# Kernel optimization log

Hardware: AMD Instinct MI355X
Metric: run time of the kernel (lower is better)

## Reference

```python
import jax, jax.numpy as jnp
import numpy as np

NY = NX = 512
DX = DY = 200.0
RHO, G, FD = 910.0, 9.81, 1e-16
TTOT, DTMAX = 200.0, 1.0
EPS = 1e-10
T_FREQ = 5.0
LAPSE = 0.006        # degC per m, lapse rate used by assumed update_smb
MELT = 0.5           # m/yr per degC, degree-day melt factor
N_STEPS = 400        # fixed upper bound on while-loop iterations (dt<=1yr, ttot=200yr)
N_PRECIP = 64


def _make_squash(scale):
    # identity in forward; backward applies atan(scale*g)/scale (torch register_hook)
    @jax.custom_vjp
    def f(x):
        return x
    def fwd(x):
        return x, None
    def bwd(_, g):
        return (jnp.arctan(scale * g) / scale,)
    f.defvjp(fwd, bwd)
    return f

squash_smb = _make_squash(0.51)   # reduce_hook
squash_zs = _make_squash(0.051)   # reduce_hook2


def update_smb(Z_surf, precip, T_m_lowest, T_s):
    # degree-day surface mass balance (update_smb not present in source excerpt)
    T = T_m_lowest[0] + T_s[0] - LAPSE * Z_surf
    return precip - MELT * jnp.maximum(T, 0.0)


def setup_inputs() -> dict:
    key = jax.random.key(0)
    k1, = jax.random.split(key, 1)
    # smooth synthetic mountain topography (Gaussian bump, 3000 m peak)
    y = np.linspace(-1.0, 1.0, NY, dtype=np.float32)
    x = np.linspace(-1.0, 1.0, NX, dtype=np.float32)
    xx, yy = np.meshgrid(x, y)
    Z_topo = jnp.asarray(3000.0 * np.exp(-(xx ** 2 + yy ** 2) / 0.3), dtype=jnp.float32)
    precip_tensor = 2.0 * jax.random.uniform(k1, (N_PRECIP, NY, NX), dtype=jnp.float32)
    T_m_lowest = jnp.array([5.0], dtype=jnp.float32)
    T_s = jnp.array([2.0], dtype=jnp.float32)
    return {"Z_topo": Z_topo, "precip_tensor": precip_tensor,
            "T_m_lowest": T_m_lowest, "T_s": T_s}


def _solve(Z_topo, precip_tensor, T_m_lowest, T_s):
    H = jnp.zeros((NY, NX), jnp.float32)
    Zs = Z_topo + H
    smb = update_smb(Zs, precip_tensor[0], T_m_lowest, T_s)
    zero2d = jnp.zeros((NY, NX), jnp.float32)
    carry0 = (H, Zs, smb, jnp.float32(0.0), jnp.int32(0), jnp.float32(0.0),
              zero2d, zero2d, jnp.bool_(False), jnp.bool_(False))

    def step(carry, _):
        H, Zs, smb, time, idx, t_last, H1, H2, s1, s2 = carry
        active = time < TTOT
        # staggered-grid SIA stencil
        H_avg = 0.25 * (H[:-1, :-1] + H[1:, 1:] + H[:-1, 1:] + H[1:, :-1])
        Sx = (Zs[:, 1:] - Zs[:, :-1]) / DX
        Sy = (Zs[1:, :] - Zs[:-1, :]) / DY
        Sx = 0.5 * (Sx[:-1, :] + Sx[1:, :])
        Sy = 0.5 * (Sy[:, :-1] + Sy[:, 1:])
        Snorm = jnp.sqrt(Sx ** 2 + Sy ** 2 + EPS)
        D = FD * (RHO * G) ** 3 * H_avg ** 5 * Snorm ** 2 + EPS   # (ny-1, nx-1)
        # dt via .item() in torch -> detached constant
        dt = jax.lax.stop_gradient(
            jnp.minimum(min(DX, DY) ** 2 / (2.7 * jnp.max(D)), DTMAX))
        dt = jnp.where(active, dt, jnp.float32(0.0))  # no-op once ttot reached
        qx = -(0.5 * (D[:-1, :] + D[1:, :])) * (Zs[1:-1, 1:] - Zs[1:-1, :-1]) / DX
        qy = -(0.5 * (D[:, :-1] + D[:, 1:])) * (Zs[1:, 1:-1] - Zs[:-1, 1:-1]) / DY
        dHdt = -(jnp.diff(qx, axis=1) / DX + jnp.diff(qy, axis=0) / DY)  # (ny-2, nx-2)
        smb_sq = squash_smb(smb)
        H = H.at[1:-1, 1:-1].add(dt * (dHdt + smb_sq[1:-1, 1:-1]))
        H = jax.nn.relu(H)
        Zs = squash_zs(Z_topo + H)
        time = time + dt
        cap1 = jnp.logical_and(jnp.logical_not(s1), time >= 120.0)
        H1 = jnp.where(cap1, jax.lax.stop_gradient(H), H1)
        s1 = jnp.logical_or(s1, cap1)
        cap2 = jnp.logical_and(jnp.logical_not(s2), time >= 160.0)
        H2 = jnp.where(cap2, jax.lax.stop_gradient(H), H2)
        s2 = jnp.logical_or(s2, cap2)
        do_upd = jnp.logical_and(active, (time - t_last) >= T_FREQ)
        idx = jnp.where(do_upd, jnp.minimum(idx + 1, N_PRECIP - 1), idx)
        smb_new = update_smb(Zs, precip_tensor[idx], T_m_lowest, T_s)
        smb = jnp.where(do_upd, smb_new, smb)
        t_last = jnp.where(do_upd, time, t_last)
        return (H, Zs, smb, time, idx, t_last, H1, H2, s1, s2), None

    carry, _ = jax.lax.scan(jax.checkpoint(step), carry0, None, length=N_STEPS)
    H, Zs, smb, time, idx, t_last, H1, H2, s1, s2 = carry
    return H1, H2, H


def reference(Z_topo, precip_tensor, T_m_lowest, T_s):
    return _solve(Z_topo, precip_tensor, T_m_lowest, T_s)
```

## Files before the change

### kernel.cpp

```cpp
#include <hip/hip_runtime.h>
#include <math.h>


#define NN 512
#define MM (NN * NN)
#define NSTEPS 400
#define NW 128
#define HR 4
#define TPB 512

typedef unsigned long long ull;

__device__ __forceinline__ ull ald(const ull* p) {
  return __hip_atomic_load(p, __ATOMIC_RELAXED, __HIP_MEMORY_SCOPE_AGENT);
}
__device__ __forceinline__ void asto(ull* p, ull v) {
  __hip_atomic_store(p, v, __ATOMIC_RELAXED, __HIP_MEMORY_SCOPE_AGENT);
}
__device__ __forceinline__ ull lld(const ull* p) {
  return __hip_atomic_load(p, __ATOMIC_RELAXED, __HIP_MEMORY_SCOPE_WORKGROUP);
}
__device__ __forceinline__ void lst(ull* p, ull v) {
  __hip_atomic_store(p, v, __ATOMIC_RELAXED, __HIP_MEMORY_SCOPE_WORKGROUP);
}

__global__ __launch_bounds__(TPB)
void glacier_kernel(const float* __restrict__ Zt,
                    const float* __restrict__ precip,
                    const float* __restrict__ Tm,
                    const float* __restrict__ Ts,
                    float* __restrict__ out,
                    ull* __restrict__ ring,
                    ull* __restrict__ halo) {
  __shared__ float Zs2[2][HR + 4][NN];
  __shared__ float DB[HR + 3][NN];
  __shared__ float HnB[HR + 2][NN];
  __shared__ ull gm[2];
  __shared__ unsigned lmx[2], lcnt[2];

  ull* upH = halo;
  ull* upD = halo + 2 * NW * NN;
  ull* dnH = halo + 4 * NW * NN;
  ull* dnD = halo + 6 * NW * NN;

  const int w = blockIdx.x;
  const int j = threadIdx.x;
  const int lane = j & 63;
  const int a = w * HR;
  const bool hasT = (w > 0), hasB = (w < NW - 1);
  const float TmTs = Tm[0] + Ts[0];
  const double RG = 910.0 * 9.81;
  const float CDIF = (float)(1e-16 * RG * RG * RG);
  const float C_Q = 1.25e-5f;
  const float C_S2 = 6.25e-6f;
  const size_t wofs = (size_t)w * NN;

  float ztreg[HR + 4];
  float hcur[HR + 2];
  float smbreg[HR + 2];

#pragma unroll
  for (int ls = 0; ls < HR + 4; ++ls) {
    int r = a - 2 + ls;
    float zt = (r >= 0 && r < NN) ? Zt[r * NN + j] : 0.f;
    ztreg[ls] = zt;
    Zs2[0][ls][j] = zt;
  }
#pragma unroll
  for (int ln = 0; ln < HR + 2; ++ln) {
    int r = a - 1 + ln;
    hcur[ln] = 0.f;
    float sm = 0.f;
    if (r >= 0 && r < NN) {
      float T = TmTs - 0.006f * ztreg[ln + 1];
      sm = precip[r * NN + j] - 0.5f * fmaxf(T, 0.f);
    }
    smbreg[ln] = sm;
  }
#pragma unroll
  for (int ld = 0; ld < HR + 3; ++ld) DB[ld][j] = 1e-10f;
#pragma unroll
  for (int rr = 0; rr < HR; ++rr) {
    int id = (a + rr) * NN + j;
    out[id] = 0.f;
    out[MM + id] = 0.f;
  }
  if (j == 0) { lmx[0] = 0u; lmx[1] = 0u; lcnt[0] = 0u; lcnt[1] = 0u;
                gm[0] = 0ull; gm[1] = 0ull; }
  float zs0r = ztreg[0], zs7r = ztreg[HR + 3];
  float d0r = 1e-10f, d6r = 1e-10f;
  const ull initD = (ull)__float_as_uint(1e-10f);
  __syncthreads();

  float time = 0.f, t_last = 0.f;
  int idx = 0;
  bool s1 = false, s2 = false;

  for (int k = 0; k < NSTEPS; ++k) {
    if (time >= 200.0f) break;

    const int p = k & 1;
    const size_t pc = (size_t)(k & 1) * NW * NN;
    const size_t pn = (size_t)((k + 1) & 1) * NW * NN;
    const ull tg = ((ull)(unsigned)(k + 1)) << 32;
    ull* ringp = ring + (size_t)(k & 1) * NW * 16;

    if (j == 0) { lmx[(k + 1) & 1] = 0u; lcnt[(k + 1) & 1] = 0u; }

    bool pre = (time - t_last) >= 4.0f;
    int idxn = min(idx + 1, 63);
    float pf[HR + 2];
    if (pre) {
      const float* prowN = precip + (size_t)idxn * MM;
#pragma unroll
      for (int ln = 0; ln < HR + 2; ++ln) {
        int i = a - 1 + ln;
        pf[ln] = (i >= 0 && i < NN) ? prowN[i * NN + j] : 0.f;
      }
    } else {
#pragma unroll
      for (int ln = 0; ln < HR + 2; ++ln) pf[ln] = 0.f;
    }
    const ull *pHt = nullptr, *pDt = nullptr, *pHb = nullptr, *pDb = nullptr;
    const ull *pDtm = nullptr, *pDbm = nullptr;
    ull vHt = 0, vDt = 0, vHb = 0, vDb = 0;
    ull vDtm = initD, vDbm = initD;
    const ull* gp = nullptr; ull gv = 0;
    if (k > 0) {
      if (hasT) {
        pHt = dnH + pc + (size_t)(w - 1) * NN + j;
        pDt = dnD + pc + (size_t)(w - 1) * NN + j;
        vHt = ald(pHt);
        if (j < NN - 1) vDt = ald(pDt);
        if (lane == 0 && j > 0) { pDtm = dnD + pc + (size_t)(w - 1) * NN + (j - 1); vDtm = ald(pDtm); }
      }
      if (hasB) {
        pHb = upH + pc + (size_t)(w + 1) * NN + j;
        pDb = upD + pc + (size_t)(w + 1) * NN + j;
        vHb = ald(pHb);
        if (j < NN - 1) vDb = ald(pDb);
        if (lane == 0 && j > 0) { pDbm = upD + pc + (size_t)(w + 1) * NN + (j - 1); vDbm = ald(pDbm); }
      }
      if (j < NW) { gp = ringp + j * 16; gv = ald(gp); }
    }
    asm volatile("" ::: "memory");

    float dHdt[HR + 2];
#pragma unroll
    for (int ln = 1; ln <= HR; ++ln) {
      int i = a - 1 + ln;
      float v = 0.f;
      if (i > 0 && i < NN - 1 && j > 0 && j < NN - 1) {
        int li = ln + 1;
        float zc = Zs2[p][li][j];
        float zw = Zs2[p][li][j - 1];
        float ze = Zs2[p][li][j + 1];
        float zn = Zs2[p][li - 1][j];
        float zs_ = Zs2[p][li + 1][j];
        float d00 = DB[ln][j - 1], d01 = DB[ln][j];
        float d10 = DB[ln + 1][j - 1], d11 = DB[ln + 1][j];
        v = C_Q * (((d01 + d11) * (ze - zc) - (d00 + d10) * (zc - zw)) +
                   ((d10 + d11) * (zs_ - zc) - (d00 + d01) * (zc - zn)));
      }
      dHdt[ln] = v;
    }

    if (k > 0) {
      if (pHt) {
        while ((unsigned)(vHt >> 32) < (unsigned)k) {
          __builtin_amdgcn_s_sleep(1); vHt = ald(pHt);
        }
        if (j < NN - 1)
          while ((unsigned)(vDt >> 32) < (unsigned)k) {
            __builtin_amdgcn_s_sleep(1); vDt = ald(pDt);
          }
        if (pDtm)
          while ((unsigned)(vDtm >> 32) < (unsigned)k) {
            __builtin_amdgcn_s_sleep(1); vDtm = ald(pDtm);
          }
        zs0r = ztreg[0] + __uint_as_float((unsigned)vHt);
        if (j < NN - 1) d0r = __uint_as_float((unsigned)vDt);
      }
      if (pHb) {
        while ((unsigned)(vHb >> 32) < (unsigned)k) {
          __builtin_amdgcn_s_sleep(1); vHb = ald(pHb);
        }
        if (j < NN - 1)
          while ((unsigned)(vDb >> 32) < (unsigned)k) {
            __builtin_amdgcn_s_sleep(1); vDb = ald(pDb);
          }
        if (pDbm)
          while ((unsigned)(vDbm >> 32) < (unsigned)k) {
            __builtin_amdgcn_s_sleep(1); vDbm = ald(pDbm);
          }
        zs7r = ztreg[HR + 3] + __uint_as_float((unsigned)vHb);
        if (j < NN - 1) d6r = __uint_as_float((unsigned)vDb);
      }
      if (j < NW) {
        while ((unsigned)(gv >> 32) < (unsigned)k) {
          __builtin_amdgcn_s_sleep(1); gv = ald(gp);
        }
        float lm = __uint_as_float((unsigned)gv);
        for (int off = 32; off; off >>= 1) lm = fmaxf(lm, __shfl_xor(lm, off));
        if (lane == 0)
          lst(&gm[j >> 6], ((ull)(unsigned)k << 32) | (ull)__float_as_uint(lm));
      }
    }

    {
      float dW0 = __shfl_up(d0r, 1);
      float dW6 = __shfl_up(d6r, 1);
      if (lane == 0) {
        dW0 = __uint_as_float((unsigned)vDtm);
        dW6 = __uint_as_float((unsigned)vDbm);
      }
      int i0 = a - 1;
      float v0 = 0.f;
      if (i0 > 0 && i0 < NN - 1 && j > 0 && j < NN - 1) {
        float zc = Zs2[p][1][j], zw = Zs2[p][1][j - 1], ze = Zs2[p][1][j + 1];
        float zn = zs0r, zs_ = Zs2[p][2][j];
        float d00 = dW0, d01 = d0r;
        float d10 = DB[1][j - 1], d11 = DB[1][j];
        v0 = C_Q * (((d01 + d11) * (ze - zc) - (d00 + d10) * (zc - zw)) +
                    ((d10 + d11) * (zs_ - zc) - (d00 + d01) * (zc - zn)));
      }
      dHdt[0] = v0;
      int i5 = a + HR;
      float v5 = 0.f;
      if (i5 > 0 && i5 < NN - 1 && j > 0 && j < NN - 1) {
        float zc = Zs2[p][HR + 2][j], zw = Zs2[p][HR + 2][j - 1], ze = Zs2[p][HR + 2][j + 1];
        float zn = Zs2[p][HR + 1][j], zs_ = zs7r;
        float d00 = DB[HR + 1][j - 1], d01 = DB[HR + 1][j];
        float d10 = dW6, d11 = d6r;
        v5 = C_Q * (((d01 + d11) * (ze - zc) - (d00 + d10) * (zc - zw)) +
                    ((d10 + d11) * (zs_ - zc) - (d00 + d01) * (zc - zn)));
      }
      dHdt[HR + 1] = v5;
    }

    float sd[HR + 2];
#pragma unroll
    for (int ln = 0; ln < HR + 2; ++ln) sd[ln] = dHdt[ln] + smbreg[ln];

    float maxD;
    if (k == 0) {
      maxD = 1e-10f;
    } else {
      ull g0 = lld(&gm[0]);
      while ((unsigned)(g0 >> 32) < (unsigned)k) {
        __builtin_amdgcn_s_sleep(1); g0 = lld(&gm[0]);
      }
      ull g1 = lld(&gm[1]);
      while ((unsigned)(g1 >> 32) < (unsigned)k) {
        __builtin_amdgcn_s_sleep(1); g1 = lld(&gm[1]);
      }
      maxD = fmaxf(__uint_as_float((unsigned)g0),
                   __uint_as_float((unsigned)g1));
    }
    float dt = fminf(40000.0f / (2.7f * maxD), 1.0f);
    float tnew = time + dt;
    bool cap1 = (!s1) && (tnew >= 120.0f);
    bool cap2 = (!s2) && (tnew >= 160.0f);
    bool do_upd = (tnew - t_last) >= 5.0f;

    float hnxt[HR + 2];
#pragma unroll
    for (int ln = 0; ln < HR + 2; ++ln) {
      int i = a - 1 + ln;
      float hnew = 0.f;
      if (i >= 0 && i < NN) {
        if (i > 0 && i < NN - 1 && j > 0 && j < NN - 1)
          hnew = fmaxf(fmaf(dt, sd[ln], hcur[ln]), 0.f);
        float zsn = ztreg[ln + 1] + hnew;
        HnB[ln][j] = hnew;
        Zs2[p ^ 1][ln + 1][j] = zsn;
        if (ln == 2) asto(upH + pn + wofs + j, tg | (ull)__float_as_uint(hnew));
        if (ln == 3) asto(dnH + pn + wofs + j, tg | (ull)__float_as_uint(hnew));
        if (i >= a && i < a + HR) {
          int id = i * NN + j;
          if (cap1) out[id] = hnew;
          if (cap2) out[MM + id] = hnew;
        }
        if (do_upd)
          smbreg[ln] = pf[ln] - 0.5f * fmaxf(TmTs - 0.006f * zsn, 0.f);
      }
      hnxt[ln] = hnew;
    }
    __syncthreads();

    float lmax = 0.f;
#pragma unroll
    for (int ln = 0; ln < HR + 1; ++ln) {
      int r = a - 1 + ln;
      if (r >= 0 && r < NN - 1 && j < NN - 1) {
        float h00 = HnB[ln][j], h01 = HnB[ln][j + 1];
        float h10 = HnB[ln + 1][j], h11 = HnB[ln + 1][j + 1];
        float z00 = Zs2[p ^ 1][ln + 1][j], z01 = Zs2[p ^ 1][ln + 1][j + 1];
        float z10 = Zs2[p ^ 1][ln + 2][j], z11 = Zs2[p ^ 1][ln + 2][j + 1];
        float havg = 0.25f * (((h00 + h11) + h01) + h10);
        float u = (z01 - z00) + (z11 - z10);
        float vv = (z10 - z00) + (z11 - z01);
        float s2 = C_S2 * (u * u + vv * vv) + 1e-10f;
        float h2 = havg * havg;
        float h4 = h2 * h2;
        float h5 = h4 * havg;
        float d = CDIF * h5 * s2 + 1e-10f;
        DB[ln + 1][j] = d;
        if (ln == 1) asto(upD + pn + wofs + j, tg | (ull)__float_as_uint(d));
        if (ln == 3) asto(dnD + pn + wofs + j, tg | (ull)__float_as_uint(d));
        lmax = fmaxf(lmax, d);
      }
    }
    for (int off = 32; off; off >>= 1) lmax = fmaxf(lmax, __shfl_xor(lmax, off));
    if (lane == 0) {
      atomicMax(&lmx[k & 1], __float_as_uint(lmax));
      unsigned c = atomicAdd(&lcnt[k & 1], 1u);
      if (c == 7u) {
        unsigned mv = atomicAdd(&lmx[k & 1], 0u);
        asto(ring + (size_t)((k + 1) & 1) * NW * 16 + w * 16,
             ((ull)(unsigned)(k + 1) << 32) | (ull)mv);
      }
    }

#pragma unroll
    for (int ln = 0; ln < HR + 2; ++ln) hcur[ln] = hnxt[ln];
    time = tnew;
    s1 = s1 || cap1;
    s2 = s2 || cap2;
    if (do_upd) { idx = idxn; t_last = tnew; }
    __syncthreads();
  }

#pragma unroll
  for (int rr = 0; rr < HR; ++rr)
    out[2 * MM + (a + rr) * NN + j] = hcur[rr + 1];
}

extern "C" void kernel_launch(void* const* d_in, const int* in_sizes, int n_in,
                              void* d_out, int out_size, void* d_ws, size_t ws_size,
                              hipStream_t stream) {
  const float* Zt = (const float*)d_in[0];
  const float* precip = (const float*)d_in[1];
  const float* Tm = (const float*)d_in[2];
  const float* Ts = (const float*)d_in[3];
  float* out = (float*)d_out;

  ull* ring = (ull*)d_ws;
  ull* halo = (ull*)((char*)d_ws + 32768);

  hipMemsetAsync(d_ws, 0, 32768 + (size_t)8 * NW * NN * sizeof(ull), stream);
  glacier_kernel<<<NW, TPB, 0, stream>>>(Zt, precip, Tm, Ts, out, ring, halo);
}
```

Baseline: 1.272 ms.

## Split each row band across two blocks with column ghost exchange

Each 4-row band is now handled by two 256-thread blocks, each owning half the columns, so the persistent kernel runs 256 blocks instead of 128 and spreads across more compute units. The blocks trade left and right ghost columns of H and D through tagged global flags with spin-waits, and the global max reduction now reads 256 ring entries. This adds cross-block synchronisation on the critical path each step, and the specL thread must wait for its neighbour's H before computing D.

```diff
diff --git a/kernel.cpp b/kernel.cpp
--- a/kernel.cpp
+++ b/kernel.cpp
@@ -5,9 +5,10 @@
 #define NN 512
 #define MM (NN * NN)
 #define NSTEPS 400
-#define NW 128
+#define NBANDS 128
+#define NBLK 256
 #define HR 4
-#define TPB 512
+#define TPB 256
 
 typedef unsigned long long ull;
 
@@ -22,6 +23,11 @@
 }
 __device__ __forceinline__ void lst(ull* p, ull v) {
   __hip_atomic_store(p, v, __ATOMIC_RELAXED, __HIP_MEMORY_SCOPE_WORKGROUP);
+}
+__device__ __forceinline__ float spinf(const ull* p, unsigned kk) {
+  ull v = ald(p);
+  while ((unsigned)(v >> 32) < kk) { __builtin_amdgcn_s_sleep(1); v = ald(p); }
+  return __uint_as_float((unsigned)v);
 }
 
 __global__ __launch_bounds__(TPB)
@@ -31,23 +37,33 @@
                     const float* __restrict__ Ts,
                     float* __restrict__ out,
                     ull* __restrict__ ring,
-                    ull* __restrict__ halo) {
-  __shared__ float Zs2[2][HR + 4][NN];
-  __shared__ float DB[HR + 3][NN];
-  __shared__ float HnB[HR + 2][NN];
-  __shared__ ull gm[2];
+                    ull* __restrict__ halo,
+                    ull* __restrict__ ghost) {
+  __shared__ float Zs2[2][HR + 4][256];
+  __shared__ float DB[HR + 3][256];
+  __shared__ float HnB[HR + 2][256];
+  __shared__ ull gm[4];
   __shared__ unsigned lmx[2], lcnt[2];
 
   ull* upH = halo;
-  ull* upD = halo + 2 * NW * NN;
-  ull* dnH = halo + 4 * NW * NN;
-  ull* dnD = halo + 6 * NW * NN;
-
-  const int w = blockIdx.x;
+  ull* upD = halo + 2 * NBANDS * NN;
+  ull* dnH = halo + 4 * NBANDS * NN;
+  ull* dnD = halo + 6 * NBANDS * NN;
+  ull* gHL = ghost;
+  ull* gDL = ghost + 2 * NBANDS * 8;
+  ull* gHR = ghost + 4 * NBANDS * 8;
+
+  const int w = blockIdx.x >> 1;
+  const int half = blockIdx.x & 1;
   const int j = threadIdx.x;
+  const int jg = (half << 8) | j;
   const int lane = j & 63;
+  const int jm = (j > 0) ? j - 1 : 0;
+  const int jp = (j < 255) ? j + 1 : 255;
   const int a = w * HR;
-  const bool hasT = (w > 0), hasB = (w < NW - 1);
+  const bool hasT = (w > 0), hasB = (w < NBANDS - 1);
+  const bool specR = (half == 1) && (j == 0);
+  const bool specL = (half == 0) && (j == 255);
   const float TmTs = Tm[0] + Ts[0];
   const double RG = 910.0 * 9.81;
   const float CDIF = (float)(1e-16 * RG * RG * RG);
@@ -62,7 +78,7 @@
 #pragma unroll
   for (int ls = 0; ls < HR + 4; ++ls) {
     int r = a - 2 + ls;
-    float zt = (r >= 0 && r < NN) ? Zt[r * NN + j] : 0.f;
+    float zt = (r >= 0 && r < NN) ? Zt[r * NN + jg] : 0.f;
     ztreg[ls] = zt;
     Zs2[0][ls][j] = zt;
   }
@@ -73,7 +89,7 @@
     float sm = 0.f;
     if (r >= 0 && r < NN) {
       float T = TmTs - 0.006f * ztreg[ln + 1];
-      sm = precip[r * NN + j] - 0.5f * fmaxf(T, 0.f);
+      sm = precip[r * NN + jg] - 0.5f * fmaxf(T, 0.f);
     }
     smbreg[ln] = sm;
   }
@@ -81,15 +97,26 @@
   for (int ld = 0; ld < HR + 3; ++ld) DB[ld][j] = 1e-10f;
 #pragma unroll
   for (int rr = 0; rr < HR; ++rr) {
-    int id = (a + rr) * NN + j;
+    int id = (a + rr) * NN + jg;
     out[id] = 0.f;
     out[MM + id] = 0.f;
   }
   if (j == 0) { lmx[0] = 0u; lmx[1] = 0u; lcnt[0] = 0u; lcnt[1] = 0u;
-                gm[0] = 0ull; gm[1] = 0ull; }
+                gm[0] = 0ull; gm[1] = 0ull; gm[2] = 0ull; gm[3] = 0ull; }
   float zs0r = ztreg[0], zs7r = ztreg[HR + 3];
   float d0r = 1e-10f, d6r = 1e-10f;
   const ull initD = (ull)__float_as_uint(1e-10f);
+  float gzt[6], gzs[6], gd[5];
+  float rzt[6], rzs[6];
+#pragma unroll
+  for (int r = 0; r < 6; ++r) {
+    int row = a - 1 + r;
+    float ztL = (specR && row >= 0 && row < NN) ? Zt[row * NN + 255] : 0.f;
+    float ztR = (specL && row >= 0 && row < NN) ? Zt[row * NN + 256] : 0.f;
+    gzt[r] = ztL; gzs[r] = ztL;
+    rzt[r] = ztR; rzs[r] = ztR;
+    if (r < 5) gd[r] = 1e-10f;
+  }
   __syncthreads();
 
   float time = 0.f, t_last = 0.f;
@@ -100,10 +127,12 @@
     if (time >= 200.0f) break;
 
     const int p = k & 1;
-    const size_t pc = (size_t)(k & 1) * NW * NN;
-    const size_t pn = (size_t)((k + 1) & 1) * NW * NN;
+    const size_t pc = (size_t)(k & 1) * NBANDS * NN;
+    const size_t pn = (size_t)((k + 1) & 1) * NBANDS * NN;
+    const size_t gpc = (size_t)(k & 1) * NBANDS * 8;
+    const size_t gpn = (size_t)((k + 1) & 1) * NBANDS * 8;
     const ull tg = ((ull)(unsigned)(k + 1)) << 32;
-    ull* ringp = ring + (size_t)(k & 1) * NW * 16;
+    ull* ringp = ring + (size_t)(k & 1) * NBLK * 16;
 
     if (j == 0) { lmx[(k + 1) & 1] = 0u; lcnt[(k + 1) & 1] = 0u; }
 
@@ -115,7 +144,7 @@
 #pragma unroll
       for (int ln = 0; ln < HR + 2; ++ln) {
         int i = a - 1 + ln;
-        pf[ln] = (i >= 0 && i < NN) ? prowN[i * NN + j] : 0.f;
+        pf[ln] = (i >= 0 && i < NN) ? prowN[i * NN + jg] : 0.f;
       }
     } else {
 #pragma unroll
@@ -125,23 +154,24 @@
     const ull *pDtm = nullptr, *pDbm = nullptr;
     ull vHt = 0, vDt = 0, vHb = 0, vDb = 0;
     ull vDtm = initD, vDbm = initD;
-    const ull* gp = nullptr; ull gv = 0;
+    const ull* gp = ringp + j * 16;
+    ull gv = 0;
     if (k > 0) {
       if (hasT) {
-        pHt = dnH + pc + (size_t)(w - 1) * NN + j;
-        pDt = dnD + pc + (size_t)(w - 1) * NN + j;
+        pHt = dnH + pc + (size_t)(w - 1) * NN + jg;
+        pDt = dnD + pc + (size_t)(w - 1) * NN + jg;
         vHt = ald(pHt);
-        if (j < NN - 1) vDt = ald(pDt);
-        if (lane == 0 && j > 0) { pDtm = dnD + pc + (size_t)(w - 1) * NN + (j - 1); vDtm = ald(pDtm); }
+        if (jg < NN - 1) vDt = ald(pDt);
+        if (lane == 0 && jg > 0) { pDtm = dnD + pc + (size_t)(w - 1) * NN + (jg - 1); vDtm = ald(pDtm); }
       }
       if (hasB) {
-        pHb = upH + pc + (size_t)(w + 1) * NN + j;
-        pDb = upD + pc + (size_t)(w + 1) * NN + j;
+        pHb = upH + pc + (size_t)(w + 1) * NN + jg;
+        pDb = upD + pc + (size_t)(w + 1) * NN + jg;
         vHb = ald(pHb);
-        if (j < NN - 1) vDb = ald(pDb);
-        if (lane == 0 && j > 0) { pDbm = upD + pc + (size_t)(w + 1) * NN + (j - 1); vDbm = ald(pDbm); }
-      }
-      if (j < NW) { gp = ringp + j * 16; gv = ald(gp); }
+        if (jg < NN - 1) vDb = ald(pDb);
+        if (lane == 0 && jg > 0) { pDbm = upD + pc + (size_t)(w + 1) * NN + (jg - 1); vDbm = ald(pDbm); }
+      }
+      gv = ald(gp);
     }
     asm volatile("" ::: "memory");
 
@@ -150,15 +180,15 @@
     for (int ln = 1; ln <= HR; ++ln) {
       int i = a - 1 + ln;
       float v = 0.f;
-      if (i > 0 && i < NN - 1 && j > 0 && j < NN - 1) {
+      if (i > 0 && i < NN - 1 && jg > 0 && jg < NN - 1 && !specR) {
         int li = ln + 1;
         float zc = Zs2[p][li][j];
-        float zw = Zs2[p][li][j - 1];
-        float ze = Zs2[p][li][j + 1];
+        float zw = Zs2[p][li][jm];
+        float ze = specL ? rzs[ln] : Zs2[p][li][jp];
         float zn = Zs2[p][li - 1][j];
         float zs_ = Zs2[p][li + 1][j];
-        float d00 = DB[ln][j - 1], d01 = DB[ln][j];
-        float d10 = DB[ln + 1][j - 1], d11 = DB[ln + 1][j];
+        float d00 = DB[ln][jm], d01 = DB[ln][j];
+        float d10 = DB[ln + 1][jm], d11 = DB[ln + 1][j];
         v = C_Q * (((d01 + d11) * (ze - zc) - (d00 + d10) * (zc - zw)) +
                    ((d10 + d11) * (zs_ - zc) - (d00 + d01) * (zc - zn)));
       }
@@ -167,44 +197,42 @@
 
     if (k > 0) {
       if (pHt) {
-        while ((unsigned)(vHt >> 32) < (unsigned)k) {
-          __builtin_amdgcn_s_sleep(1); vHt = ald(pHt);
+        while ((unsigned)(vHt >> 32) < (unsigned)k) { __builtin_amdgcn_s_sleep(1); vHt = ald(pHt); }
+        if (jg < NN - 1)
+          while ((unsigned)(vDt >> 32) < (unsigned)k) { __builtin_amdgcn_s_sleep(1); vDt = ald(pDt); }
+        if (pDtm)
+          while ((unsigned)(vDtm >> 32) < (unsigned)k) { __builtin_amdgcn_s_sleep(1); vDtm = ald(pDtm); }
+        zs0r = ztreg[0] + __uint_as_float((unsigned)vHt);
+        if (jg < NN - 1) d0r = __uint_as_float((unsigned)vDt);
+      }
+      if (pHb) {
+        while ((unsigned)(vHb >> 32) < (unsigned)k) { __builtin_amdgcn_s_sleep(1); vHb = ald(pHb); }
+        if (jg < NN - 1)
+          while ((unsigned)(vDb >> 32) < (unsigned)k) { __builtin_amdgcn_s_sleep(1); vDb = ald(pDb); }
+        if (pDbm)
+          while ((unsigned)(vDbm >> 32) < (unsigned)k) { __builtin_amdgcn_s_sleep(1); vDbm = ald(pDbm); }
+        zs7r = ztreg[HR + 3] + __uint_as_float((unsigned)vHb);
+        if (jg < NN - 1) d6r = __uint_as_float((unsigned)vDb);
+      }
+      if (specR) {
+        const ull* hb = gHL + gpc + (size_t)w * 8;
+        const ull* db = gDL + gpc + (size_t)w * 8;
+#pragma unroll
+        for (int r = 0; r < 6; ++r) {
+          int row = a - 1 + r;
+          if (row >= 0 && row < NN) gzs[r] = gzt[r] + spinf(hb + r, (unsigned)k);
         }
-        if (j < NN - 1)
-          while ((unsigned)(vDt >> 32) < (unsigned)k) {
-            __builtin_amdgcn_s_sleep(1); vDt = ald(pDt);
-          }
-        if (pDtm)
-          while ((unsigned)(vDtm >> 32) < (unsigned)k) {
-            __builtin_amdgcn_s_sleep(1); vDtm = ald(pDtm);
-          }
-        zs0r = ztreg[0] + __uint_as_float((unsigned)vHt);
-        if (j < NN - 1) d0r = __uint_as_float((unsigned)vDt);
-      }
-      if (pHb) {
-        while ((unsigned)(vHb >> 32) < (unsigned)k) {
-          __builtin_amdgcn_s_sleep(1); vHb = ald(pHb);
+#pragma unroll
+        for (int r = 0; r < 5; ++r) {
+          int row = a - 1 + r;
+          if (row >= 0 && row < NN - 1) gd[r] = spinf(db + r, (unsigned)k);
         }
-        if (j < NN - 1)
-          while ((unsigned)(vDb >> 32) < (unsigned)k) {
-            __builtin_amdgcn_s_sleep(1); vDb = ald(pDb);
-          }
-        if (pDbm)
-          while ((unsigned)(vDbm >> 32) < (unsigned)k) {
-            __builtin_amdgcn_s_sleep(1); vDbm = ald(pDbm);
-          }
-        zs7r = ztreg[HR + 3] + __uint_as_float((unsigned)vHb);
-        if (j < NN - 1) d6r = __uint_as_float((unsigned)vDb);
-      }
-      if (j < NW) {
-        while ((unsigned)(gv >> 32) < (unsigned)k) {
-          __builtin_amdgcn_s_sleep(1); gv = ald(gp);
-        }
-        float lm = __uint_as_float((unsigned)gv);
-        for (int off = 32; off; off >>= 1) lm = fmaxf(lm, __shfl_xor(lm, off));
-        if (lane == 0)
-          lst(&gm[j >> 6], ((ull)(unsigned)k << 32) | (ull)__float_as_uint(lm));
-      }
+      }
+      while ((unsigned)(gv >> 32) < (unsigned)k) { __builtin_amdgcn_s_sleep(1); gv = ald(gp); }
+      float lm = __uint_as_float((unsigned)gv);
+      for (int off = 32; off; off >>= 1) lm = fmaxf(lm, __shfl_xor(lm, off));
+      if (lane == 0)
+        lst(&gm[j >> 6], ((ull)(unsigned)k << 32) | (ull)__float_as_uint(lm));
     }
 
     {
@@ -216,26 +244,50 @@
       }
       int i0 = a - 1;
       float v0 = 0.f;
-      if (i0 > 0 && i0 < NN - 1 && j > 0 && j < NN - 1) {
-        float zc = Zs2[p][1][j], zw = Zs2[p][1][j - 1], ze = Zs2[p][1][j + 1];
+      if (i0 > 0 && i0 < NN - 1 && jg > 0 && jg < NN - 1 && !specR) {
+        float zc = Zs2[p][1][j], zw = Zs2[p][1][jm];
+        float ze = specL ? rzs[0] : Zs2[p][1][jp];
         float zn = zs0r, zs_ = Zs2[p][2][j];
         float d00 = dW0, d01 = d0r;
-        float d10 = DB[1][j - 1], d11 = DB[1][j];
+        float d10 = DB[1][jm], d11 = DB[1][j];
         v0 = C_Q * (((d01 + d11) * (ze - zc) - (d00 + d10) * (zc - zw)) +
                     ((d10 + d11) * (zs_ - zc) - (d00 + d01) * (zc - zn)));
       }
       dHdt[0] = v0;
       int i5 = a + HR;
       float v5 = 0.f;
-      if (i5 > 0 && i5 < NN - 1 && j > 0 && j < NN - 1) {
-        float zc = Zs2[p][HR + 2][j], zw = Zs2[p][HR + 2][j - 1], ze = Zs2[p][HR + 2][j + 1];
+      if (i5 > 0 && i5 < NN - 1 && jg > 0 && jg < NN - 1 && !specR) {
+        float zc = Zs2[p][HR + 2][j], zw = Zs2[p][HR + 2][jm];
+        float ze = specL ? rzs[5] : Zs2[p][HR + 2][jp];
         float zn = Zs2[p][HR + 1][j], zs_ = zs7r;
-        float d00 = DB[HR + 1][j - 1], d01 = DB[HR + 1][j];
+        float d00 = DB[HR + 1][jm], d01 = DB[HR + 1][j];
         float d10 = dW6, d11 = d6r;
         v5 = C_Q * (((d01 + d11) * (ze - zc) - (d00 + d10) * (zc - zw)) +
                     ((d10 + d11) * (zs_ - zc) - (d00 + d01) * (zc - zn)));
       }
       dHdt[HR + 1] = v5;
+      if (specR) {
+#pragma unroll
+        for (int ln = 0; ln < HR + 2; ++ln) {
+          int i = a - 1 + ln;
+          float v = 0.f;
+          if (i > 0 && i < NN - 1) {
+            int li = ln + 1;
+            float zc = Zs2[p][li][0];
+            float ze = Zs2[p][li][1];
+            float zn = (ln == 0) ? zs0r : Zs2[p][li - 1][0];
+            float zs_ = (ln == HR + 1) ? zs7r : Zs2[p][li + 1][0];
+            float zw = gzs[ln];
+            float d01 = (ln == 0) ? d0r : DB[ln][0];
+            float d11 = (ln == HR + 1) ? d6r : DB[ln + 1][0];
+            float d00 = (ln == 0) ? dW0 : gd[ln - 1];
+            float d10 = (ln == HR + 1) ? dW6 : gd[ln];
+            v = C_Q * (((d01 + d11) * (ze - zc) - (d00 + d10) * (zc - zw)) +
+                       ((d10 + d11) * (zs_ - zc) - (d00 + d01) * (zc - zn)));
+          }
+          dHdt[ln] = v;
+        }
+      }
     }
 
     float sd[HR + 2];
@@ -246,16 +298,13 @@
     if (k == 0) {
       maxD = 1e-10f;
     } else {
-      ull g0 = lld(&gm[0]);
-      while ((unsigned)(g0 >> 32) < (unsigned)k) {
-        __builtin_amdgcn_s_sleep(1); g0 = lld(&gm[0]);
-      }
-      ull g1 = lld(&gm[1]);
-      while ((unsigned)(g1 >> 32) < (unsigned)k) {
-        __builtin_amdgcn_s_sleep(1); g1 = lld(&gm[1]);
-      }
-      maxD = fmaxf(__uint_as_float((unsigned)g0),
-                   __uint_as_float((unsigned)g1));
+      maxD = 0.f;
+#pragma unroll
+      for (int q = 0; q < 4; ++q) {
+        ull g = lld(&gm[q]);
+        while ((unsigned)(g >> 32) < (unsigned)k) { __builtin_amdgcn_s_sleep(1); g = lld(&gm[q]); }
+        maxD = fmaxf(maxD, __uint_as_float((unsigned)g));
+      }
     }
     float dt = fminf(40000.0f / (2.7f * maxD), 1.0f);
     float tnew = time + dt;
@@ -269,15 +318,17 @@
       int i = a - 1 + ln;
       float hnew = 0.f;
       if (i >= 0 && i < NN) {
-        if (i > 0 && i < NN - 1 && j > 0 && j < NN - 1)
+        if (i > 0 && i < NN - 1 && jg > 0 && jg < NN - 1)
           hnew = fmaxf(fmaf(dt, sd[ln], hcur[ln]), 0.f);
         float zsn = ztreg[ln + 1] + hnew;
         HnB[ln][j] = hnew;
         Zs2[p ^ 1][ln + 1][j] = zsn;
-        if (ln == 2) asto(upH + pn + wofs + j, tg | (ull)__float_as_uint(hnew));
-        if (ln == 3) asto(dnH + pn + wofs + j, tg | (ull)__float_as_uint(hnew));
+        if (ln == 2) asto(upH + pn + wofs + jg, tg | (ull)__float_as_uint(hnew));
+        if (ln == 3) asto(dnH + pn + wofs + jg, tg | (ull)__float_as_uint(hnew));
+        if (specL) asto(gHL + gpn + (size_t)w * 8 + ln, tg | (ull)__float_as_uint(hnew));
+        if (specR) asto(gHR + gpn + (size_t)w * 8 + ln, tg | (ull)__float_as_uint(hnew));
         if (i >= a && i < a + HR) {
-          int id = i * NN + j;
+          int id = i * NN + jg;
           if (cap1) out[id] = hnew;
           if (cap2) out[MM + id] = hnew;
         }
@@ -288,15 +339,32 @@
     }
     __syncthreads();
 
+    float rhn[6] = {0.f, 0.f, 0.f, 0.f, 0.f, 0.f};
+    if (specL) {
+      const ull* hb = gHR + gpn + (size_t)w * 8;
+#pragma unroll
+      for (int r = 0; r < 6; ++r) {
+        int row = a - 1 + r;
+        if (row >= 0 && row < NN) {
+          rhn[r] = spinf(hb + r, (unsigned)(k + 1));
+          rzs[r] = rzt[r] + rhn[r];
+        }
+      }
+    }
+
     float lmax = 0.f;
 #pragma unroll
     for (int ln = 0; ln < HR + 1; ++ln) {
       int r = a - 1 + ln;
-      if (r >= 0 && r < NN - 1 && j < NN - 1) {
-        float h00 = HnB[ln][j], h01 = HnB[ln][j + 1];
-        float h10 = HnB[ln + 1][j], h11 = HnB[ln + 1][j + 1];
-        float z00 = Zs2[p ^ 1][ln + 1][j], z01 = Zs2[p ^ 1][ln + 1][j + 1];
-        float z10 = Zs2[p ^ 1][ln + 2][j], z11 = Zs2[p ^ 1][ln + 2][j + 1];
+      if (r >= 0 && r < NN - 1 && jg < NN - 1) {
+        float h00 = HnB[ln][j];
+        float h01 = specL ? rhn[ln] : HnB[ln][jp];
+        float h10 = HnB[ln + 1][j];
+        float h11 = specL ? rhn[ln + 1] : HnB[ln + 1][jp];
+        float z00 = Zs2[p ^ 1][ln + 1][j];
+        float z01 = specL ? rzs[ln] : Zs2[p ^ 1][ln + 1][jp];
+        float z10 = Zs2[p ^ 1][ln + 2][j];
+        float z11 = specL ? rzs[ln + 1] : Zs2[p ^ 1][ln + 2][jp];
         float havg = 0.25f * (((h00 + h11) + h01) + h10);
         float u = (z01 - z00) + (z11 - z10);
         float vv = (z10 - z00) + (z11 - z01);
@@ -306,8 +374,9 @@
         float h5 = h4 * havg;
         float d = CDIF * h5 * s2 + 1e-10f;
         DB[ln + 1][j] = d;
-        if (ln == 1) asto(upD + pn + wofs + j, tg | (ull)__float_as_uint(d));
-        if (ln == 3) asto(dnD + pn + wofs + j, tg | (ull)__float_as_uint(d));
+        if (ln == 1) asto(upD + pn + wofs + jg, tg | (ull)__float_as_uint(d));
+        if (ln == 3) asto(dnD + pn + wofs + jg, tg | (ull)__float_as_uint(d));
+        if (specL) asto(gDL + gpn + (size_t)w * 8 + ln, tg | (ull)__float_as_uint(d));
         lmax = fmaxf(lmax, d);
       }
     }
@@ -315,9 +384,9 @@
     if (lane == 0) {
       atomicMax(&lmx[k & 1], __float_as_uint(lmax));
       unsigned c = atomicAdd(&lcnt[k & 1], 1u);
-      if (c == 7u) {
+      if (c == 3u) {
         unsigned mv = atomicAdd(&lmx[k & 1], 0u);
-        asto(ring + (size_t)((k + 1) & 1) * NW * 16 + w * 16,
+        asto(ring + (size_t)((k + 1) & 1) * NBLK * 16 + (size_t)blockIdx.x * 16,
              ((ull)(unsigned)(k + 1) << 32) | (ull)mv);
       }
     }
@@ -333,7 +402,7 @@
 
 #pragma unroll
   for (int rr = 0; rr < HR; ++rr)
-    out[2 * MM + (a + rr) * NN + j] = hcur[rr + 1];
+    out[2 * MM + (a + rr) * NN + jg] = hcur[rr + 1];
 }
 
 extern "C" void kernel_launch(void* const* d_in, const int* in_sizes, int n_in,
@@ -346,8 +415,10 @@
   float* out = (float*)d_out;
 
   ull* ring = (ull*)d_ws;
-  ull* halo = (ull*)((char*)d_ws + 32768);
-
-  hipMemsetAsync(d_ws, 0, 32768 + (size_t)8 * NW * NN * sizeof(ull), stream);
-  glacier_kernel<<<NW, TPB, 0, stream>>>(Zt, precip, Tm, Ts, out, ring, halo);
-}
+  ull* halo = (ull*)((char*)d_ws + 65536);
+  ull* ghost = (ull*)((char*)d_ws + 65536 + 4194304);
+
+  hipMemsetAsync(d_ws, 0, 65536 + 4194304 + 49152, stream);
+  glacier_kernel<<<NBLK, TPB, 0, stream>>>(Zt, precip, Tm, Ts, out,
+                                           ring, halo, ghost);
+}
```

After: 3.069 ms. 2.41x slower.
